# Performance work log

Measured on AMD Instinct MI355X. Metric: run time of the kernel, lower is better.

Reference implementation:

```python
import jax, jax.numpy as jnp
import numpy as np

B, S, H = 2, 256, 512
EPS = 1e-12  # TPLinker conditional LayerNorm default epsilon
NEG = -1e30  # finite stand-in for -inf in running max


def _cond_layer_norm(x, cond, Wg, Wb, gamma, beta):
    # TPLinker conditional LayerNorm: gamma/beta are modulated by a linear map of cond.
    g = gamma + cond @ Wg          # (..., H)
    b = beta + cond @ Wb           # (..., H)
    xc = x - jnp.mean(x, axis=-1, keepdims=True)
    inv = jax.lax.rsqrt(jnp.mean(xc * xc, axis=-1, keepdims=True) + EPS)
    return xc * inv * g + b


def setup_inputs() -> dict:
    key = jax.random.key(0)
    ks = jax.random.split(key, 6)
    return {
        "seq_hiddens": jax.random.normal(ks[0], (B, S, H), jnp.float32),
        "mask": jnp.ones((B, S), jnp.float32),
        "lamtha": jax.random.uniform(ks[1], (H,), jnp.float32),
        "Wg1": jax.random.normal(ks[2], (H, H), jnp.float32) * 0.02,
        "Wb1": jax.random.normal(ks[3], (H, H), jnp.float32) * 0.02,
        "g1": jnp.ones((H,), jnp.float32),
        "b1": jnp.zeros((H,), jnp.float32),
        "Wg2": jax.random.normal(ks[4], (H, H), jnp.float32) * 0.02,
        "Wb2": jax.random.normal(ks[5], (H, H), jnp.float32) * 0.02,
        "g2": jnp.ones((H,), jnp.float32),
        "b2": jnp.zeros((H,), jnp.float32),
    }


def reference(seq_hiddens, mask, lamtha, Wg1, Wb1, g1, b1, Wg2, Wb2, g2, b2):
    # mask additive penalty, broadcast over hidden (matches (1-mask)*-1000 expand)
    seq = seq_hiddens + ((1.0 - mask) * -1000.0)[:, :, None]  # (B,S,H)

    ii, jj = jnp.triu_indices(S)  # row-major pairs (i, j>=i), same order as the torch loop

    # window means over seq[i..j] via cumulative sums (replaces O(S^3) recomputation)
    csum = jnp.cumsum(seq, axis=1)                              # (B,S,H)
    lens = (jj - ii + 1).astype(seq.dtype)[None, :, None]
    mean_pairs = (csum[:, jj] - csum[:, ii] + seq[:, ii]) / lens  # (B,P,H)

    # window maxes over seq[i..j]: scan over j keeping running max per start i
    idx = jnp.arange(S)

    def step(state, j):
        sj = jnp.take(seq, j, axis=1)  # (B,H)
        new = jnp.where((idx <= j)[None, :, None],
                        jnp.maximum(state, sj[:, None, :]),
                        jnp.asarray(NEG, seq.dtype))
        return new, new

    _, Mall = jax.lax.scan(step, jnp.full((B, S, H), NEG, seq.dtype), idx)  # (S_j,B,S_i,H)
    max_pairs = Mall[jj, :, ii].transpose(1, 0, 2)  # (B,P,H)

    # mix pooling
    inner = lamtha * mean_pairs + (1.0 - lamtha) * max_pairs  # (B,P,H)

    visible = seq[:, jj]  # (B,P,H) token j
    repeat = seq[:, ii]   # (B,P,H) token i

    shaking = _cond_layer_norm(visible, repeat, Wg1, Wb1, g1, b1)
    return _cond_layer_norm(shaking, inner, Wg2, Wb2, g2, b2)
```

## Files before the change

### kernel.cpp

```cpp
#include <hip/hip_runtime.h>
#include <hip/hip_bf16.h>

typedef __hip_bfloat16 bf16;
typedef short short8 __attribute__((ext_vector_type(8)));
typedef float floatx4 __attribute__((ext_vector_type(4)));

#define S 256
#define H 512
#define P 32896
#define NROWS 65792
#define NEGF -1e30f
#define EPSF 1e-12f

#define OFF_LN1    2129920u
#define OFF_G1     3178496u
#define OFF_B1     4227072u
#define OFF_WCAT   5275648u
#define OFF_II     6324224u
#define OFF_JJ     6390016u
#define OFF_MU2    6455808u
#define OFF_INV2   6718976u
#define OFF_INNER  6982144u

__device__ __forceinline__ void gld_lds16(const void* g, void* l) {
    __builtin_amdgcn_global_load_lds(
        (const __attribute__((address_space(1))) void*)g,
        (__attribute__((address_space(3))) void*)l, 16, 0, 0);
}

__global__ __launch_bounds__(512) void fusedA_kernel(
    const float* __restrict__ x, const float* __restrict__ mask,
    float* __restrict__ ln1,
    const float* __restrict__ Wg2, const float* __restrict__ Wb2,
    bf16* __restrict__ wcatT,
    unsigned short* __restrict__ ii, unsigned short* __restrict__ jj) {
    __shared__ float part[8][8][2];
    __shared__ float rstat[8][2];
    if (blockIdx.x < 64) {
        int b = blockIdx.x >> 5, sc = blockIdx.x & 31, h = threadIdx.x;
        int wave = h >> 6, lane = h & 63;
        int s0 = sc * 8;
        float v[8];
#pragma unroll
        for (int t = 0; t < 8; ++t) {
            int s = s0 + t;
            v[t] = x[(size_t)(b * S + s) * H + h] + (1.0f - mask[b * S + s]) * (-1000.0f);
        }
#pragma unroll
        for (int t = 0; t < 8; ++t) {
            float s = v[t], q = v[t] * v[t];
            for (int o = 1; o < 64; o <<= 1) { s += __shfl_xor(s, o); q += __shfl_xor(q, o); }
            if (lane == 0) { part[wave][t][0] = s; part[wave][t][1] = q; }
        }
        __syncthreads();
        if (h < 16) {
            int row = h >> 1, st = h & 1;
            float a = 0.0f;
#pragma unroll
            for (int w = 0; w < 8; ++w) a += part[w][row][st];
            rstat[row][st] = a;
        }
        __syncthreads();
#pragma unroll
        for (int t = 0; t < 8; ++t) {
            float m = rstat[t][0] * (1.0f / 512.0f);
            float var = rstat[t][1] * (1.0f / 512.0f) - m * m;
            var = var < 0.0f ? 0.0f : var;
            float inv = rsqrtf(var + EPSF);
            ln1[(size_t)(b * S + s0 + t) * H + h] = (v[t] - m) * inv;
        }
    } else {
        int n = blockIdx.x - 64;
        if (n < 1024) {
            int k = threadIdx.x;
            int tt = n >> 7, c = n & 127;
            int h = tt * 64 + (c & 63);
            float v = (c < 64) ? Wg2[(size_t)k * H + h] : Wb2[(size_t)k * H + h];
            wcatT[(size_t)n * H + k] = __float2bfloat16(v);
        } else {
            int p = (n - 1024) * 512 + threadIdx.x;
            if (p >= P) return;
            float disc = 513.0f * 513.0f - 8.0f * (float)p;
            int i = (int)((513.0f - sqrtf(disc)) * 0.5f);
            i = i < 0 ? 0 : (i > S - 1 ? S - 1 : i);
            while (i > 0 && (i * S - i * (i - 1) / 2) > p) --i;
            while (i < S - 1 && ((i + 1) * S - (i + 1) * i / 2) <= p) ++i;
            int off = i * S - i * (i - 1) / 2;
            ii[p] = (unsigned short)i;
            jj[p] = (unsigned short)(i + (p - off));
        }
    }
}

__global__ __launch_bounds__(256) void g1b1_kernel(
    const float* __restrict__ x, const float* __restrict__ mask,
    const float* __restrict__ Wg1, const float* __restrict__ Wb1,
    const float* __restrict__ g1, const float* __restrict__ b1,
    float* __restrict__ G1, float* __restrict__ B1) {
    __shared__ float rowbuf[4][H];
    int grp = blockIdx.x;
    int mat = blockIdx.y;
    int tid = threadIdx.x;
    int h0 = tid, h1 = tid + 256;
    int r0 = grp * 4;
#pragma unroll
    for (int r = 0; r < 4; ++r) {
        int row = r0 + r;
        float add = (1.0f - mask[row]) * (-1000.0f);
        rowbuf[r][h0] = x[(size_t)row * H + h0] + add;
        rowbuf[r][h1] = x[(size_t)row * H + h1] + add;
    }
    __syncthreads();
    const float* W = mat ? Wb1 : Wg1;
    float acc[4][2] = {{0, 0}, {0, 0}, {0, 0}, {0, 0}};
#pragma unroll 2
    for (int k4 = 0; k4 < 128; ++k4) {
        float4 a0 = ((const float4*)rowbuf[0])[k4];
        float4 a1 = ((const float4*)rowbuf[1])[k4];
        float4 a2 = ((const float4*)rowbuf[2])[k4];
        float4 a3 = ((const float4*)rowbuf[3])[k4];
        float w00 = W[(size_t)(k4 * 4 + 0) * H + h0], w01 = W[(size_t)(k4 * 4 + 0) * H + h1];
        float w10 = W[(size_t)(k4 * 4 + 1) * H + h0], w11 = W[(size_t)(k4 * 4 + 1) * H + h1];
        float w20 = W[(size_t)(k4 * 4 + 2) * H + h0], w21 = W[(size_t)(k4 * 4 + 2) * H + h1];
        float w30 = W[(size_t)(k4 * 4 + 3) * H + h0], w31 = W[(size_t)(k4 * 4 + 3) * H + h1];
        acc[0][0] += a0.x * w00 + a0.y * w10 + a0.z * w20 + a0.w * w30;
        acc[0][1] += a0.x * w01 + a0.y * w11 + a0.z * w21 + a0.w * w31;
        acc[1][0] += a1.x * w00 + a1.y * w10 + a1.z * w20 + a1.w * w30;
        acc[1][1] += a1.x * w01 + a1.y * w11 + a1.z * w21 + a1.w * w31;
        acc[2][0] += a2.x * w00 + a2.y * w10 + a2.z * w20 + a2.w * w30;
        acc[2][1] += a2.x * w01 + a2.y * w11 + a2.z * w21 + a2.w * w31;
        acc[3][0] += a3.x * w00 + a3.y * w10 + a3.z * w20 + a3.w * w30;
        acc[3][1] += a3.x * w01 + a3.y * w11 + a3.z * w21 + a3.w * w31;
    }
    float bias0 = (mat ? b1 : g1)[h0];
    float bias1 = (mat ? b1 : g1)[h1];
    float* dst = mat ? B1 : G1;
#pragma unroll
    for (int r = 0; r < 4; ++r) {
        dst[(size_t)(r0 + r) * H + h0] = acc[r][0] + bias0;
        dst[(size_t)(r0 + r) * H + h1] = acc[r][1] + bias1;
    }
}

__global__ __launch_bounds__(256) void innerstats_kernel(
    const float* __restrict__ x, const float* __restrict__ mask,
    const float* __restrict__ lamtha,
    const float* __restrict__ ln1, const float* __restrict__ G1,
    const float* __restrict__ B1,
    bf16* __restrict__ inner, float* __restrict__ mu2, float* __restrict__ inv2) {
    __shared__ float maskadd[256];
    int id = blockIdx.x;
    int kind = id & 1, sub = id >> 1;
    int t = sub & 255, b = sub >> 8;
    int i = b ? (255 - t) : t;
    int tid = threadIdx.x;
    int off = i * S - i * (i - 1) / 2;

    if (kind == 0) {
        int h2 = tid;
        maskadd[tid] = (1.0f - mask[b * S + tid]) * (-1000.0f);
        __syncthreads();
        float2 lam = ((const float2*)lamtha)[h2];
        float2 oml = {1.0f - lam.x, 1.0f - lam.y};
        const float2* xb = (const float2*)(x + (size_t)b * S * H);
        float2 mrun = {NEGF, NEGF};
        float2 srun = {0.0f, 0.0f};
        size_t base = (size_t)b * P + (size_t)off;
        __hip_bfloat162* dst = (__hip_bfloat162*)inner;
        int j = i;
#define INNER_STEP(xx, jx)                                                 \
    {                                                                      \
        float ma = maskadd[jx];                                            \
        float vx = xx.x + ma, vy = xx.y + ma;                              \
        srun.x += vx;                                                      \
        srun.y += vy;                                                      \
        mrun.x = fmaxf(mrun.x, vx);                                        \
        mrun.y = fmaxf(mrun.y, vy);                                        \
        float rl = 1.0f / (float)((jx) - i + 1);                           \
        float mx = srun.x * rl;                                            \
        float my = srun.y * rl;                                            \
        __hip_bfloat162 o;                                                 \
        o.x = __float2bfloat16(lam.x * mx + oml.x * mrun.x);               \
        o.y = __float2bfloat16(lam.y * my + oml.y * mrun.y);               \
        dst[(base + (size_t)((jx) - i)) * 256 + h2] = o;                   \
    }
        for (; j + 4 <= S; j += 4) {
            float2 x0 = xb[(j + 0) * 256 + h2];
            float2 x1 = xb[(j + 1) * 256 + h2];
            float2 x2 = xb[(j + 2) * 256 + h2];
            float2 x3 = xb[(j + 3) * 256 + h2];
            INNER_STEP(x0, j + 0)
            INNER_STEP(x1, j + 1)
            INNER_STEP(x2, j + 2)
            INNER_STEP(x3, j + 3)
        }
        for (; j < S; ++j) {
            float2 xv = xb[j * 256 + h2];
            INNER_STEP(xv, j)
        }
#undef INNER_STEP
    } else {
        int wave = tid >> 6, lane = tid & 63;
        const float4* gp = (const float4*)(G1 + (size_t)(b * S + i) * H);
        const float4* bp = (const float4*)(B1 + (size_t)(b * S + i) * H);
        float4 ga = gp[lane * 2], gb = gp[lane * 2 + 1];
        float4 ba = bp[lane * 2], bb = bp[lane * 2 + 1];
        for (int j = i + wave; j < S; j += 4) {
            const float4* lp = (const float4*)(ln1 + (size_t)(b * S + j) * H);
            float4 a0 = lp[lane * 2], a1 = lp[lane * 2 + 1];
            float v0 = a0.x * ga.x + ba.x, v1 = a0.y * ga.y + ba.y;
            float v2 = a0.z * ga.z + ba.z, v3 = a0.w * ga.w + ba.w;
            float v4 = a1.x * gb.x + bb.x, v5 = a1.y * gb.y + bb.y;
            float v6 = a1.z * gb.z + bb.z, v7 = a1.w * gb.w + bb.w;
            float sum = ((v0 + v1) + (v2 + v3)) + ((v4 + v5) + (v6 + v7));
            float ss = ((v0 * v0 + v1 * v1) + (v2 * v2 + v3 * v3)) +
                       ((v4 * v4 + v5 * v5) + (v6 * v6 + v7 * v7));
            for (int o = 1; o < 64; o <<= 1) { sum += __shfl_xor(sum, o); ss += __shfl_xor(ss, o); }
            if (lane == 0) {
                int r = b * P + off + (j - i);
                float m = sum * (1.0f / 512.0f);
                float var = ss * (1.0f / 512.0f) - m * m;
                var = var < 0.0f ? 0.0f : var;
                mu2[r] = m;
                inv2[r] = rsqrtf(var + EPSF);
            }
        }
    }
}

__global__ __launch_bounds__(256, 2) void gemm_kernel(
    const bf16* __restrict__ inner, const bf16* __restrict__ wcatT,
    const float* __restrict__ g2, const float* __restrict__ b2,
    const float* __restrict__ ln1, const float* __restrict__ G1, const float* __restrict__ B1,
    const unsigned short* __restrict__ ii, const unsigned short* __restrict__ jj,
    const float* __restrict__ mu2, const float* __restrict__ inv2,
    float* __restrict__ out) {
    extern __shared__ __align__(16) char smem[];

    const int tid = threadIdx.x;
    const int wave = tid >> 6, lane = tid & 63;
    const int q = lane >> 4, l15 = lane & 15;
    const int wm = wave & 1, wn = wave >> 1;

    const int id = blockIdx.x;
    int rb, t;
    if (id < 4096) { rb = (id >> 6) * 8 + (id & 7); t = (id >> 3) & 7; }
    else           { int w = id - 4096; rb = 512 + (w & 1); t = w >> 1; }
    const int R0 = rb * 128;

    const int srow = tid >> 3;
    const int sx8 = ((tid & 7) ^ (srow & 7)) * 8;
    const bf16* const Ag = inner + (size_t)(R0 + srow) * H + sx8;
    const bf16* const Bg = wcatT + (size_t)(t * 128 + srow) * H + sx8;

    char* const A0 = smem;
    char* const B0 = smem + 16384;
    char* const A1 = smem + 32768;
    char* const B1s = smem + 49152;

    floatx4 acc[4][4];
#pragma unroll
    for (int a = 0; a < 4; ++a)
#pragma unroll
        for (int c = 0; c < 4; ++c) acc[a][c] = (floatx4){0.f, 0.f, 0.f, 0.f};

    auto STAGE = [&](int kt, char* Ad, char* Bd) {
#pragma unroll
        for (int i2 = 0; i2 < 4; ++i2)
            gld_lds16(Ag + (size_t)i2 * 32 * H + kt * 64, Ad + i2 * 4096 + wave * 1024);
#pragma unroll
        for (int i2 = 0; i2 < 4; ++i2)
            gld_lds16(Bg + (size_t)i2 * 32 * H + kt * 64, Bd + i2 * 4096 + wave * 1024);
    };

    STAGE(0, A0, B0);
    STAGE(1, A1, B1s);
    asm volatile("s_waitcnt vmcnt(8)" ::: "memory");
    asm volatile("s_barrier" ::: "memory");

#pragma unroll
    for (int kt = 0; kt < 8; ++kt) {
        char* const As = (kt & 1) ? A1 : A0;
        char* const Bs = (kt & 1) ? B1s : B0;

        short8 bfr[4][2], af[4][2];
#pragma unroll
        for (int ks = 0; ks < 2; ++ks) {
#pragma unroll
            for (int fn = 0; fn < 4; ++fn) {
                int nr = (fn < 2 ? wn * 32 + fn * 16 : 64 + wn * 32 + (fn - 2) * 16) + l15;
                bfr[fn][ks] = *(const short8*)(Bs + nr * 128 + (((ks * 4 + q) ^ (l15 & 7)) << 4));
            }
#pragma unroll
            for (int fm = 0; fm < 4; ++fm) {
                int mr = wm * 64 + fm * 16 + l15;
                af[fm][ks] = *(const short8*)(As + mr * 128 + (((ks * 4 + q) ^ (l15 & 7)) << 4));
            }
        }

        __builtin_amdgcn_s_setprio(1);
#pragma unroll
        for (int fm = 0; fm < 4; ++fm)
#pragma unroll
            for (int fn = 0; fn < 4; ++fn)
                acc[fm][fn] = __builtin_amdgcn_mfma_f32_16x16x32_bf16(af[fm][0], bfr[fn][0], acc[fm][fn], 0, 0, 0);
        __builtin_amdgcn_s_setprio(0);

        if (kt < 6) {
            asm volatile("s_waitcnt lgkmcnt(0)" ::: "memory");
            asm volatile("s_barrier" ::: "memory");
            STAGE(kt + 2, As, Bs);
        }

        __builtin_amdgcn_s_setprio(1);
#pragma unroll
        for (int fm = 0; fm < 4; ++fm)
#pragma unroll
            for (int fn = 0; fn < 4; ++fn)
                acc[fm][fn] = __builtin_amdgcn_mfma_f32_16x16x32_bf16(af[fm][1], bfr[fn][1], acc[fm][fn], 0, 0, 0);
        __builtin_amdgcn_s_setprio(0);

        if (kt < 6) {
            asm volatile("s_waitcnt vmcnt(8)" ::: "memory");
            asm volatile("s_barrier" ::: "memory");
        } else if (kt == 6) {
            asm volatile("s_waitcnt vmcnt(0)" ::: "memory");
            asm volatile("s_barrier" ::: "memory");
        }
    }

    float g2v[2], b2v[2];
#pragma unroll
    for (int fg = 0; fg < 2; ++fg) {
        int h = t * 64 + wn * 32 + fg * 16 + l15;
        g2v[fg] = g2[h];
        b2v[fg] = b2[h];
    }
#pragma unroll
    for (int fm = 0; fm < 4; ++fm) {
#pragma unroll
        for (int r = 0; r < 4; ++r) {
            int m = wm * 64 + fm * 16 + q * 4 + r;
            int rg = R0 + m;
            int b = (rg >= P) ? 1 : 0;
            int p = rg - b * P;
            int i = ii[p], j = jj[p];
            float mu = mu2[rg], iv = inv2[rg];
            const float* lp = ln1 + (size_t)(b * S + j) * H + t * 64 + wn * 32;
            const float* gp = G1 + (size_t)(b * S + i) * H + t * 64 + wn * 32;
            const float* bp = B1 + (size_t)(b * S + i) * H + t * 64 + wn * 32;
            float* op = out + (size_t)rg * H + t * 64 + wn * 32;
#pragma unroll
            for (int fg = 0; fg < 2; ++fg) {
                int c = fg * 16 + l15;
                float s = (lp[c] * gp[c] + bp[c] - mu) * iv;
                float G2v = acc[fm][fg][r] + g2v[fg];
                float B2v = acc[fm][fg + 2][r] + b2v[fg];
                op[c] = s * G2v + B2v;
            }
        }
    }
}

extern "C" void kernel_launch(void* const* d_in, const int* in_sizes, int n_in,
                              void* d_out, int out_size, void* d_ws, size_t ws_size,
                              hipStream_t stream) {
    const float* x = (const float*)d_in[0];
    const float* mask = (const float*)d_in[1];
    const float* lamtha = (const float*)d_in[2];
    const float* Wg1 = (const float*)d_in[3];
    const float* Wb1 = (const float*)d_in[4];
    const float* g1 = (const float*)d_in[5];
    const float* b1 = (const float*)d_in[6];
    const float* Wg2 = (const float*)d_in[7];
    const float* Wb2 = (const float*)d_in[8];
    const float* g2 = (const float*)d_in[9];
    const float* b2 = (const float*)d_in[10];
    float* out = (float*)d_out;

    char* ws = (char*)d_ws;
    float* ln1 = (float*)(ws + OFF_LN1);
    float* G1 = (float*)(ws + OFF_G1);
    float* B1 = (float*)(ws + OFF_B1);
    bf16* wcatT = (bf16*)(ws + OFF_WCAT);
    unsigned short* iiA = (unsigned short*)(ws + OFF_II);
    unsigned short* jjA = (unsigned short*)(ws + OFF_JJ);
    float* mu2 = (float*)(ws + OFF_MU2);
    float* inv2 = (float*)(ws + OFF_INV2);
    bf16* inner = (bf16*)(ws + OFF_INNER);

    static bool attr_set = false;
    if (!attr_set) {
        hipFuncSetAttribute((const void*)gemm_kernel,
                            hipFuncAttributeMaxDynamicSharedMemorySize, 65536);
        attr_set = true;
    }

    hipLaunchKernelGGL(fusedA_kernel, dim3(1153), dim3(512), 0, stream,
                       x, mask, ln1, Wg2, Wb2, wcatT, iiA, jjA);
    hipLaunchKernelGGL(g1b1_kernel, dim3(128, 2), dim3(256), 0, stream,
                       x, mask, Wg1, Wb1, g1, b1, G1, B1);
    hipLaunchKernelGGL(innerstats_kernel, dim3(1024), dim3(256), 0, stream,
                       x, mask, lamtha, ln1, G1, B1, inner, mu2, inv2);
    hipLaunchKernelGGL(gemm_kernel, dim3(4112), dim3(256), 65536, stream,
                       inner, wcatT, g2, b2, ln1, G1, B1, iiA, jjA, mu2, inv2, out);
}
```

Before: 301.5 us.

## Unroll cond-GEMV and inner-pool loops, peel last GEMM tile to prefetch epilogue indices

```diff
diff --git a/kernel.cpp b/kernel.cpp
--- a/kernel.cpp
+++ b/kernel.cpp
@@ -113,24 +113,30 @@
     __syncthreads();
     const float* W = mat ? Wb1 : Wg1;
     float acc[4][2] = {{0, 0}, {0, 0}, {0, 0}, {0, 0}};
-#pragma unroll 2
-    for (int k4 = 0; k4 < 128; ++k4) {
-        float4 a0 = ((const float4*)rowbuf[0])[k4];
-        float4 a1 = ((const float4*)rowbuf[1])[k4];
-        float4 a2 = ((const float4*)rowbuf[2])[k4];
-        float4 a3 = ((const float4*)rowbuf[3])[k4];
-        float w00 = W[(size_t)(k4 * 4 + 0) * H + h0], w01 = W[(size_t)(k4 * 4 + 0) * H + h1];
-        float w10 = W[(size_t)(k4 * 4 + 1) * H + h0], w11 = W[(size_t)(k4 * 4 + 1) * H + h1];
-        float w20 = W[(size_t)(k4 * 4 + 2) * H + h0], w21 = W[(size_t)(k4 * 4 + 2) * H + h1];
-        float w30 = W[(size_t)(k4 * 4 + 3) * H + h0], w31 = W[(size_t)(k4 * 4 + 3) * H + h1];
-        acc[0][0] += a0.x * w00 + a0.y * w10 + a0.z * w20 + a0.w * w30;
-        acc[0][1] += a0.x * w01 + a0.y * w11 + a0.z * w21 + a0.w * w31;
-        acc[1][0] += a1.x * w00 + a1.y * w10 + a1.z * w20 + a1.w * w30;
-        acc[1][1] += a1.x * w01 + a1.y * w11 + a1.z * w21 + a1.w * w31;
-        acc[2][0] += a2.x * w00 + a2.y * w10 + a2.z * w20 + a2.w * w30;
-        acc[2][1] += a2.x * w01 + a2.y * w11 + a2.z * w21 + a2.w * w31;
-        acc[3][0] += a3.x * w00 + a3.y * w10 + a3.z * w20 + a3.w * w30;
-        acc[3][1] += a3.x * w01 + a3.y * w11 + a3.z * w21 + a3.w * w31;
+    for (int k8 = 0; k8 < 64; ++k8) {
+        float4 ra[4][2];
+#pragma unroll
+        for (int r = 0; r < 4; ++r) {
+            ra[r][0] = ((const float4*)rowbuf[r])[k8 * 2];
+            ra[r][1] = ((const float4*)rowbuf[r])[k8 * 2 + 1];
+        }
+        float w0[8], w1[8];
+#pragma unroll
+        for (int kk = 0; kk < 8; ++kk) {
+            w0[kk] = W[(size_t)(k8 * 8 + kk) * H + h0];
+            w1[kk] = W[(size_t)(k8 * 8 + kk) * H + h1];
+        }
+#pragma unroll
+        for (int r = 0; r < 4; ++r) {
+            acc[r][0] += ra[r][0].x * w0[0] + ra[r][0].y * w0[1] +
+                         ra[r][0].z * w0[2] + ra[r][0].w * w0[3] +
+                         ra[r][1].x * w0[4] + ra[r][1].y * w0[5] +
+                         ra[r][1].z * w0[6] + ra[r][1].w * w0[7];
+            acc[r][1] += ra[r][0].x * w1[0] + ra[r][0].y * w1[1] +
+                         ra[r][0].z * w1[2] + ra[r][0].w * w1[3] +
+                         ra[r][1].x * w1[4] + ra[r][1].y * w1[5] +
+                         ra[r][1].z * w1[6] + ra[r][1].w * w1[7];
+        }
     }
     float bias0 = (mat ? b1 : g1)[h0];
     float bias1 = (mat ? b1 : g1)[h1];
@@ -148,7 +154,8 @@
     const float* __restrict__ ln1, const float* __restrict__ G1,
     const float* __restrict__ B1,
     bf16* __restrict__ inner, float* __restrict__ mu2, float* __restrict__ inv2) {
-    __shared__ float maskadd[256];
+    __shared__ float sh_a[256];
+    __shared__ float sh_b[256];
     int id = blockIdx.x;
     int kind = id & 1, sub = id >> 1;
     int t = sub & 255, b = sub >> 8;
@@ -158,7 +165,8 @@
 
     if (kind == 0) {
         int h2 = tid;
-        maskadd[tid] = (1.0f - mask[b * S + tid]) * (-1000.0f);
+        sh_a[tid] = (1.0f - mask[b * S + tid]) * (-1000.0f);
+        sh_b[tid] = 1.0f / (float)(tid + 1);
         __syncthreads();
         float2 lam = ((const float2*)lamtha)[h2];
         float2 oml = {1.0f - lam.x, 1.0f - lam.y};
@@ -170,20 +178,36 @@
         int j = i;
 #define INNER_STEP(xx, jx)                                                 \
     {                                                                      \
-        float ma = maskadd[jx];                                            \
+        float ma = sh_a[jx];                                               \
         float vx = xx.x + ma, vy = xx.y + ma;                              \
         srun.x += vx;                                                      \
         srun.y += vy;                                                      \
         mrun.x = fmaxf(mrun.x, vx);                                        \
         mrun.y = fmaxf(mrun.y, vy);                                        \
-        float rl = 1.0f / (float)((jx) - i + 1);                           \
-        float mx = srun.x * rl;                                            \
-        float my = srun.y * rl;                                            \
-        __hip_bfloat162 o;                                                 \
-        o.x = __float2bfloat16(lam.x * mx + oml.x * mrun.x);               \
-        o.y = __float2bfloat16(lam.y * my + oml.y * mrun.y);               \
-        dst[(base + (size_t)((jx) - i)) * 256 + h2] = o;                   \
-    }
+        float rl = sh_b[(jx) - i];                                         \
+        float fx = lam.x * (srun.x * rl) + oml.x * mrun.x;                 \
+        float fy = lam.y * (srun.y * rl) + oml.y * mrun.y;                 \
+        dst[(base + (size_t)((jx) - i)) * 256 + h2] =                      \
+            __float22bfloat162_rn(make_float2(fx, fy));                    \
+    }
+        for (; j + 8 <= S; j += 8) {
+            float2 x0 = xb[(j + 0) * 256 + h2];
+            float2 x1 = xb[(j + 1) * 256 + h2];
+            float2 x2 = xb[(j + 2) * 256 + h2];
+            float2 x3 = xb[(j + 3) * 256 + h2];
+            float2 x4 = xb[(j + 4) * 256 + h2];
+            float2 x5 = xb[(j + 5) * 256 + h2];
+            float2 x6 = xb[(j + 6) * 256 + h2];
+            float2 x7 = xb[(j + 7) * 256 + h2];
+            INNER_STEP(x0, j + 0)
+            INNER_STEP(x1, j + 1)
+            INNER_STEP(x2, j + 2)
+            INNER_STEP(x3, j + 3)
+            INNER_STEP(x4, j + 4)
+            INNER_STEP(x5, j + 5)
+            INNER_STEP(x6, j + 6)
+            INNER_STEP(x7, j + 7)
+        }
         for (; j + 4 <= S; j += 4) {
             float2 x0 = xb[(j + 0) * 256 + h2];
             float2 x1 = xb[(j + 1) * 256 + h2];
@@ -279,7 +303,7 @@
     asm volatile("s_barrier" ::: "memory");
 
 #pragma unroll
-    for (int kt = 0; kt < 8; ++kt) {
+    for (int kt = 0; kt < 7; ++kt) {
         char* const As = (kt & 1) ? A1 : A0;
         char* const Bs = (kt & 1) ? B1s : B0;
 
@@ -323,19 +347,14 @@
         if (kt < 6) {
             asm volatile("s_waitcnt vmcnt(8)" ::: "memory");
             asm volatile("s_barrier" ::: "memory");
-        } else if (kt == 6) {
+        } else {
             asm volatile("s_waitcnt vmcnt(0)" ::: "memory");
             asm volatile("s_barrier" ::: "memory");
         }
     }
 
-    float g2v[2], b2v[2];
-#pragma unroll
-    for (int fg = 0; fg < 2; ++fg) {
-        int h = t * 64 + wn * 32 + fg * 16 + l15;
-        g2v[fg] = g2[h];
-        b2v[fg] = b2[h];
-    }
+    int ipre[4][4], jpre[4][4];
+    float mupre[4][4], ivpre[4][4];
 #pragma unroll
     for (int fm = 0; fm < 4; ++fm) {
 #pragma unroll
@@ -344,8 +363,57 @@
             int rg = R0 + m;
             int b = (rg >= P) ? 1 : 0;
             int p = rg - b * P;
-            int i = ii[p], j = jj[p];
-            float mu = mu2[rg], iv = inv2[rg];
+            ipre[fm][r] = ii[p];
+            jpre[fm][r] = jj[p];
+            mupre[fm][r] = mu2[rg];
+            ivpre[fm][r] = inv2[rg];
+        }
+    }
+
+    {
+        char* const As = A1;
+        char* const Bs = B1s;
+        short8 bfr[4][2], af[4][2];
+#pragma unroll
+        for (int ks = 0; ks < 2; ++ks) {
+#pragma unroll
+            for (int fn = 0; fn < 4; ++fn) {
+                int nr = (fn < 2 ? wn * 32 + fn * 16 : 64 + wn * 32 + (fn - 2) * 16) + l15;
+                bfr[fn][ks] = *(const short8*)(Bs + nr * 128 + (((ks * 4 + q) ^ (l15 & 7)) << 4));
+            }
+#pragma unroll
+            for (int fm = 0; fm < 4; ++fm) {
+                int mr = wm * 64 + fm * 16 + l15;
+                af[fm][ks] = *(const short8*)(As + mr * 128 + (((ks * 4 + q) ^ (l15 & 7)) << 4));
+            }
+        }
+        __builtin_amdgcn_s_setprio(1);
+#pragma unroll
+        for (int ks = 0; ks < 2; ++ks)
+#pragma unroll
+            for (int fm = 0; fm < 4; ++fm)
+#pragma unroll
+                for (int fn = 0; fn < 4; ++fn)
+                    acc[fm][fn] = __builtin_amdgcn_mfma_f32_16x16x32_bf16(af[fm][ks], bfr[fn][ks], acc[fm][fn], 0, 0, 0);
+        __builtin_amdgcn_s_setprio(0);
+    }
+
+    float g2v[2], b2v[2];
+#pragma unroll
+    for (int fg = 0; fg < 2; ++fg) {
+        int h = t * 64 + wn * 32 + fg * 16 + l15;
+        g2v[fg] = g2[h];
+        b2v[fg] = b2[h];
+    }
+#pragma unroll
+    for (int fm = 0; fm < 4; ++fm) {
+#pragma unroll
+        for (int r = 0; r < 4; ++r) {
+            int m = wm * 64 + fm * 16 + q * 4 + r;
+            int rg = R0 + m;
+            int b = (rg >= P) ? 1 : 0;
+            int i = ipre[fm][r], j = jpre[fm][r];
+            float mu = mupre[fm][r], iv = ivpre[fm][r];
             const float* lp = ln1 + (size_t)(b * S + j) * H + t * 64 + wn * 32;
             const float* gp = G1 + (size_t)(b * S + i) * H + t * 64 + wn * 32;
             const float* bp = B1 + (size_t)(b * S + i) * H + t * 64 + wn * 32;
```

After: 298.0 us, median of 2. Within noise of the previous version (-1.2%).
